# Performance work log

Hardware: AMD Instinct MI355X
Metric: run time of the kernel (lower is better)

## Reference

```python
import jax, jax.numpy as jnp
import numpy as np

B, S, H, NH = 2, 2048, 2048, 16
HD = H // NH
SCALE = 1.0 / np.sqrt(HD).astype(np.float32)


def setup_inputs() -> dict:
    key = jax.random.key(0)
    ks = jax.random.split(key, 11)
    std = 1.0 / np.sqrt(H)
    inp = {
        'query': jax.random.normal(ks[0], (B, S, H), dtype=jnp.float32),
        'key': jax.random.normal(ks[1], (B, S, H), dtype=jnp.float32),
        'value': jax.random.normal(ks[2], (B, S, H), dtype=jnp.float32),
        'Wq': jax.random.normal(ks[3], (H, H), dtype=jnp.float32) * std,
        'bq': jax.random.normal(ks[4], (H,), dtype=jnp.float32) * std,
        'Wk': jax.random.normal(ks[5], (H, H), dtype=jnp.float32) * std,
        'bk': jax.random.normal(ks[6], (H,), dtype=jnp.float32) * std,
        'Wv': jax.random.normal(ks[7], (H, H), dtype=jnp.float32) * std,
        'bv': jax.random.normal(ks[8], (H,), dtype=jnp.float32) * std,
        'Wo': jax.random.normal(ks[9], (H, H), dtype=jnp.float32) * std,
        'bo': jax.random.normal(ks[10], (H,), dtype=jnp.float32) * std,
    }
    return inp


def reference(query, key, value, Wq, bq, Wk, bk, Wv, bv, Wo, bo):
    # Linear projections (torch Linear: x @ W.T + b)
    q = query @ Wq.T + bq
    k = key @ Wk.T + bk
    v = value @ Wv.T + bv
    # [B, NH, S, HD]
    q = q.reshape(B, S, NH, HD).transpose(0, 2, 1, 3)
    k = k.reshape(B, S, NH, HD).transpose(0, 2, 1, 3)
    v = v.reshape(B, S, NH, HD).transpose(0, 2, 1, 3)
    scores = jnp.einsum('bhqd,bhkd->bhqk', q, k) * SCALE
    attn = jax.nn.softmax(scores, axis=-1)  # dropout p=0 (eval)
    ctx = jnp.einsum('bhqk,bhkd->bhqd', attn, v)
    ctx = ctx.transpose(0, 2, 1, 3).reshape(B, S, H)
    out = ctx @ Wo.T + bo
    return out
```

## Files before the change

kernel.cpp:

```cpp
#include <hip/hip_runtime.h>


typedef __bf16 bf16_t;
typedef __bf16 bf16x8 __attribute__((ext_vector_type(8)));
typedef float  f32x4  __attribute__((ext_vector_type(4)));

#define DEVI __device__ __forceinline__

DEVI void async_copy16(const void* gsrc, void* ldst) {
  __builtin_amdgcn_global_load_lds(
      (const __attribute__((address_space(1))) unsigned int*)gsrc,
      (__attribute__((address_space(3))) unsigned int*)ldst, 16, 0, 0);
}

constexpr int Bc = 2, Sc = 2048, Hc = 2048, NHc = 16, HDc = 128;
constexpr float SCALE_F = 0.088388347648318447f;
constexpr int PSTR = 72;

DEVI void cast_body(const float* __restrict__ in, bf16_t* __restrict__ out) {
  int i = (blockIdx.x * 256 + threadIdx.x) * 8;
  float4 f0 = *(const float4*)(in + i);
  float4 f1 = *(const float4*)(in + i + 4);
  union { bf16_t h[8]; uint4 u; } o;
  o.h[0] = (bf16_t)f0.x; o.h[1] = (bf16_t)f0.y;
  o.h[2] = (bf16_t)f0.z; o.h[3] = (bf16_t)f0.w;
  o.h[4] = (bf16_t)f1.x; o.h[5] = (bf16_t)f1.y;
  o.h[6] = (bf16_t)f1.z; o.h[7] = (bf16_t)f1.w;
  *(uint4*)(out + i) = o.u;
}

__global__ void cast3(const float* __restrict__ a, const float* __restrict__ b,
                      const float* __restrict__ c, bf16_t* __restrict__ oa,
                      bf16_t* __restrict__ ob, bf16_t* __restrict__ oc) {
  const float* src = blockIdx.y == 0 ? a : blockIdx.y == 1 ? b : c;
  bf16_t* dst = blockIdx.y == 0 ? oa : blockIdx.y == 1 ? ob : oc;
  cast_body(src, dst);
}

__global__ void cast4(const float* __restrict__ a, const float* __restrict__ b,
                      const float* __restrict__ c, const float* __restrict__ d,
                      bf16_t* __restrict__ oa, bf16_t* __restrict__ ob,
                      bf16_t* __restrict__ oc, bf16_t* __restrict__ od) {
  const float* src = blockIdx.y == 0 ? a : blockIdx.y == 1 ? b
                   : blockIdx.y == 2 ? c : d;
  bf16_t* dst = blockIdx.y == 0 ? oa : blockIdx.y == 1 ? ob
              : blockIdx.y == 2 ? oc : od;
  cast_body(src, dst);
}

template <int M, int N, int K, int OUT_MODE>
__global__ __launch_bounds__(256, 2) void gemm_bt(const bf16_t* __restrict__ A,
                                                  const bf16_t* __restrict__ Bw,
                                                  const float* __restrict__ bias,
                                                  void* __restrict__ Cout,
                                                  float scale) {
  constexpr int BM = 128, BN = 128, BK = 64;
  __shared__ __align__(16) bf16_t As[BM * BK];
  __shared__ __align__(16) bf16_t Bs[BN * BK];
  const int tid = threadIdx.x;
  const int lane = tid & 63;
  const int wave = tid >> 6;
  const int bm = blockIdx.x & (M / BM - 1);
  const int bn = blockIdx.x / (M / BM);
  const int wm = wave >> 1, wn = wave & 1;
  const int quad = lane >> 4, l15 = lane & 15;

  int s_r[4], s_c[4];
#pragma unroll
  for (int i = 0; i < 4; ++i) {
    int seg = wave * 4 + i;
    int r = seg * 8 + (lane >> 3);
    s_r[i] = r;
    s_c[i] = (lane & 7) ^ (r & 7);
  }
  const bf16_t* Abase = A + (size_t)bm * BM * K;
  const bf16_t* Bbase = Bw + (size_t)bn * BN * K;

  f32x4 zero4 = {0.f, 0.f, 0.f, 0.f};
  f32x4 acc[4][4];
#pragma unroll
  for (int i = 0; i < 4; ++i)
#pragma unroll
    for (int j = 0; j < 4; ++j) acc[i][j] = zero4;

  int arow[4], brow[4];
#pragma unroll
  for (int t = 0; t < 4; ++t) {
    arow[t] = wm * 64 + t * 16 + l15;
    brow[t] = wn * 64 + t * 16 + l15;
  }

  for (int kt = 0; kt < K / BK; ++kt) {
    const int k0 = kt * BK;
#pragma unroll
    for (int i = 0; i < 4; ++i) {
      int seg = wave * 4 + i;
      async_copy16(Abase + (size_t)s_r[i] * K + k0 + s_c[i] * 8, As + seg * 512);
      async_copy16(Bbase + (size_t)s_r[i] * K + k0 + s_c[i] * 8, Bs + seg * 512);
    }
    __syncthreads();
#pragma unroll
    for (int ks = 0; ks < 2; ++ks) {
      bf16x8 af[4], bfv[4];
#pragma unroll
      for (int mt = 0; mt < 4; ++mt)
        af[mt] = *(const bf16x8*)(As + arow[mt] * 64 +
                                  (((ks * 4 + quad) ^ (arow[mt] & 7)) * 8));
#pragma unroll
      for (int nt = 0; nt < 4; ++nt)
        bfv[nt] = *(const bf16x8*)(Bs + brow[nt] * 64 +
                                   (((ks * 4 + quad) ^ (brow[nt] & 7)) * 8));
#pragma unroll
      for (int mt = 0; mt < 4; ++mt)
#pragma unroll
        for (int nt = 0; nt < 4; ++nt)
          acc[mt][nt] = __builtin_amdgcn_mfma_f32_16x16x32_bf16(
              af[mt], bfv[nt], acc[mt][nt], 0, 0, 0);
    }
    __syncthreads();
  }

  float bv[4];
#pragma unroll
  for (int nt = 0; nt < 4; ++nt) bv[nt] = bias[bn * BN + brow[nt]];

#pragma unroll
  for (int mt = 0; mt < 4; ++mt) {
    const int rbase = bm * BM + wm * 64 + mt * 16 + quad * 4;
#pragma unroll
    for (int nt = 0; nt < 4; ++nt) {
      const int col = bn * BN + brow[nt];
      if constexpr (OUT_MODE == 0) {
        bf16_t* C = (bf16_t*)Cout;
#pragma unroll
        for (int r = 0; r < 4; ++r)
          C[(size_t)(rbase + r) * N + col] = (bf16_t)((acc[mt][nt][r] + bv[nt]) * scale);
      } else if constexpr (OUT_MODE == 2) {
        float* C = (float*)Cout;
#pragma unroll
        for (int r = 0; r < 4; ++r)
          C[(size_t)(rbase + r) * N + col] = acc[mt][nt][r] + bv[nt];
      } else {
        bf16_t* C = (bf16_t*)Cout;
        const int bb = rbase >> 11;
        const int s0 = rbase & (Sc - 1);
        const int h = col >> 7, d = col & (HDc - 1);
        union { bf16_t h4[4]; uint2 u; } o;
#pragma unroll
        for (int r = 0; r < 4; ++r) o.h4[r] = (bf16_t)(acc[mt][nt][r] + bv[nt]);
        *(uint2*)(C + (((size_t)(bb * NHc + h) * HDc + d) * Sc + s0)) = o.u;
      }
    }
  }
}

__global__ __launch_bounds__(256, 2) void flash_attn(const bf16_t* __restrict__ Q,
                                                     const bf16_t* __restrict__ Kg,
                                                     const bf16_t* __restrict__ Vt,
                                                     bf16_t* __restrict__ ctx) {
  __shared__ __align__(16) bf16_t smem[64 * 128 + 128 * 64 + 4 * 32 * PSTR];
  bf16_t* Ks = smem;
  bf16_t* Vs = smem + 8192;
  bf16_t* Ps = smem + 16384;

  const int tid = threadIdx.x, lane = tid & 63, wave = tid >> 6;
  const int quad = lane >> 4, l15 = lane & 15;
  const int bid = blockIdx.x;
  const int qt = bid & 15, h = (bid >> 4) & 15, b = bid >> 8;

  bf16_t* Pw = Ps + wave * (32 * PSTR);

  bf16x8 qf[2][4];
#pragma unroll
  for (int mt = 0; mt < 2; ++mt) {
    int grow = b * Sc + qt * 128 + wave * 32 + mt * 16 + l15;
    const bf16_t* qp = Q + (size_t)grow * Hc + h * HDc;
#pragma unroll
    for (int kc = 0; kc < 4; ++kc) qf[mt][kc] = *(const bf16x8*)(qp + kc * 32 + quad * 8);
  }

  f32x4 zero4 = {0.f, 0.f, 0.f, 0.f};
  f32x4 o[2][8];
#pragma unroll
  for (int mt = 0; mt < 2; ++mt)
#pragma unroll
    for (int dt = 0; dt < 8; ++dt) o[mt][dt] = zero4;
  float mrow[2][4], lrow[2][4];
#pragma unroll
  for (int mt = 0; mt < 2; ++mt)
#pragma unroll
    for (int r = 0; r < 4; ++r) { mrow[mt][r] = -1e30f; lrow[mt][r] = 0.f; }

  int kr_[4], kc_[4], vr_[4], vc_[4];
#pragma unroll
  for (int i = 0; i < 4; ++i) {
    int s = wave * 4 + i;
    kr_[i] = s * 4 + quad;        kc_[i] = l15 ^ (kr_[i] & 7);
    vr_[i] = s * 8 + (lane >> 3); vc_[i] = (lane & 7) ^ (vr_[i] & 7);
  }
  const bf16_t* Kbase = Kg + (size_t)b * Sc * Hc + h * HDc;
  const bf16_t* Vbase = Vt + (size_t)(b * NHc + h) * HDc * Sc;

  for (int kb = 0; kb < 32; ++kb) {
#pragma unroll
    for (int i = 0; i < 4; ++i) {
      int s = wave * 4 + i;
      async_copy16(Kbase + (size_t)(kb * 64 + kr_[i]) * Hc + kc_[i] * 8, Ks + s * 512);
      async_copy16(Vbase + (size_t)vr_[i] * Sc + kb * 64 + vc_[i] * 8, Vs + s * 512);
    }
    __syncthreads();

    f32x4 sf[2][4];
#pragma unroll
    for (int mt = 0; mt < 2; ++mt)
#pragma unroll
      for (int nt = 0; nt < 4; ++nt) sf[mt][nt] = zero4;
#pragma unroll
    for (int kc = 0; kc < 4; ++kc)
#pragma unroll
      for (int nt = 0; nt < 4; ++nt) {
        int kr = nt * 16 + l15;
        bf16x8 kf = *(const bf16x8*)(Ks + kr * 128 + (((kc * 4 + quad) ^ (kr & 7)) * 8));
        sf[0][nt] = __builtin_amdgcn_mfma_f32_16x16x32_bf16(qf[0][kc], kf, sf[0][nt], 0, 0, 0);
        sf[1][nt] = __builtin_amdgcn_mfma_f32_16x16x32_bf16(qf[1][kc], kf, sf[1][nt], 0, 0, 0);
      }

#pragma unroll
    for (int mt = 0; mt < 2; ++mt)
#pragma unroll
      for (int r = 0; r < 4; ++r) {
        float mx = sf[mt][0][r];
#pragma unroll
        for (int nt = 1; nt < 4; ++nt) mx = fmaxf(mx, sf[mt][nt][r]);
#pragma unroll
        for (int off = 1; off < 16; off <<= 1) mx = fmaxf(mx, __shfl_xor(mx, off));
        float mnew = fmaxf(mrow[mt][r], mx);
        float alpha = __expf(mrow[mt][r] - mnew);
        float rs = 0.f;
#pragma unroll
        for (int nt = 0; nt < 4; ++nt) {
          float p = __expf(sf[mt][nt][r] - mnew);
          sf[mt][nt][r] = p;
          rs += p;
        }
#pragma unroll
        for (int off = 1; off < 16; off <<= 1) rs += __shfl_xor(rs, off);
        lrow[mt][r] = lrow[mt][r] * alpha + rs;
        mrow[mt][r] = mnew;
#pragma unroll
        for (int dt = 0; dt < 8; ++dt) o[mt][dt][r] *= alpha;
      }

#pragma unroll
    for (int mt = 0; mt < 2; ++mt)
#pragma unroll
      for (int nt = 0; nt < 4; ++nt)
#pragma unroll
        for (int r = 0; r < 4; ++r)
          Pw[(mt * 16 + quad * 4 + r) * PSTR + nt * 16 + l15] = (bf16_t)sf[mt][nt][r];

    bf16x8 pf[2][2];
#pragma unroll
    for (int mt = 0; mt < 2; ++mt) {
      const bf16_t* pr = Pw + (mt * 16 + l15) * PSTR;
#pragma unroll
      for (int kc = 0; kc < 2; ++kc)
        pf[mt][kc] = *(const bf16x8*)(pr + kc * 32 + quad * 8);
    }

#pragma unroll
    for (int kc = 0; kc < 2; ++kc)
#pragma unroll
      for (int dt = 0; dt < 8; ++dt) {
        int vr = dt * 16 + l15;
        bf16x8 vf = *(const bf16x8*)(Vs + vr * 64 + (((kc * 4 + quad) ^ (vr & 7)) * 8));
        o[0][dt] = __builtin_amdgcn_mfma_f32_16x16x32_bf16(pf[0][kc], vf, o[0][dt], 0, 0, 0);
        o[1][dt] = __builtin_amdgcn_mfma_f32_16x16x32_bf16(pf[1][kc], vf, o[1][dt], 0, 0, 0);
      }
    __syncthreads();
  }

  __syncthreads();
  bf16_t* Ow = smem + wave * 4096;
#pragma unroll
  for (int mt = 0; mt < 2; ++mt) {
    float rinv[4];
#pragma unroll
    for (int r = 0; r < 4; ++r) rinv[r] = 1.f / lrow[mt][r];
#pragma unroll
    for (int dt = 0; dt < 8; ++dt)
#pragma unroll
      for (int r = 0; r < 4; ++r)
        Ow[(mt * 16 + quad * 4 + r) * 128 + dt * 16 + l15] = (bf16_t)(o[mt][dt][r] * rinv[r]);
  }
#pragma unroll
  for (int r = 0; r < 32; ++r) {
    unsigned v = *(const unsigned*)(Ow + r * 128 + lane * 2);
    int grow = b * Sc + qt * 128 + wave * 32 + r;
    *(unsigned*)(ctx + (size_t)grow * Hc + h * HDc + lane * 2) = v;
  }
}

extern "C" void kernel_launch(void* const* d_in, const int* in_sizes, int n_in,
                              void* d_out, int out_size, void* d_ws, size_t ws_size,
                              hipStream_t stream) {
  const float* query = (const float*)d_in[0];
  const float* key_i = (const float*)d_in[1];
  const float* value = (const float*)d_in[2];
  const float* Wq = (const float*)d_in[3];
  const float* bq = (const float*)d_in[4];
  const float* Wk = (const float*)d_in[5];
  const float* bk = (const float*)d_in[6];
  const float* Wv = (const float*)d_in[7];
  const float* bv = (const float*)d_in[8];
  const float* Wo = (const float*)d_in[9];
  const float* bo = (const float*)d_in[10];

  const size_t XE = (size_t)Bc * Sc * Hc;
  const size_t WE = (size_t)Hc * Hc;
  const size_t need = 6 * XE * 2 + 4 * WE * 2;
  if (ws_size < need) return;

  char* ws = (char*)d_ws;
  size_t off = 0;
  auto alloc = [&](size_t bytes) {
    char* p = ws + off;
    off += (bytes + 255) & ~(size_t)255;
    return p;
  };
  bf16_t* Xq = (bf16_t*)alloc(XE * 2);
  bf16_t* Xk = (bf16_t*)alloc(XE * 2);
  bf16_t* Xv = (bf16_t*)alloc(XE * 2);
  bf16_t* Wqb = (bf16_t*)alloc(WE * 2);
  bf16_t* Wkb = (bf16_t*)alloc(WE * 2);
  bf16_t* Wvb = (bf16_t*)alloc(WE * 2);
  bf16_t* Wob = (bf16_t*)alloc(WE * 2);
  bf16_t* qb = (bf16_t*)alloc(XE * 2);
  bf16_t* kb = (bf16_t*)alloc(XE * 2);
  bf16_t* vtb = (bf16_t*)alloc(XE * 2);
  bf16_t* ctxb = Xq;

  cast3<<<dim3((unsigned)(XE / 2048), 3), 256, 0, stream>>>(query, key_i, value, Xq, Xk, Xv);
  cast4<<<dim3((unsigned)(WE / 2048), 4), 256, 0, stream>>>(Wq, Wk, Wv, Wo, Wqb, Wkb, Wvb, Wob);

  gemm_bt<4096, 2048, 2048, 0><<<512, 256, 0, stream>>>(Xq, Wqb, bq, qb, SCALE_F);
  gemm_bt<4096, 2048, 2048, 0><<<512, 256, 0, stream>>>(Xk, Wkb, bk, kb, 1.0f);
  gemm_bt<4096, 2048, 2048, 1><<<512, 256, 0, stream>>>(Xv, Wvb, bv, vtb, 1.0f);

  flash_attn<<<512, 256, 0, stream>>>(qb, kb, vtb, ctxb);

  gemm_bt<4096, 2048, 2048, 2><<<512, 256, 0, stream>>>(ctxb, Wob, bo, (float*)d_out, 1.0f);
}
```

Baseline: 479.0 us.

## Pipeline projection GEMMs with triple-buffered LDS and larger 256x128 tiles

```diff
diff --git a/kernel.cpp b/kernel.cpp
--- a/kernel.cpp
+++ b/kernel.cpp
@@ -49,14 +49,16 @@
 }
 
 template <int M, int N, int K, int OUT_MODE>
-__global__ __launch_bounds__(256, 2) void gemm_bt(const bf16_t* __restrict__ A,
+__global__ __launch_bounds__(512, 2) void gemm_bt(const bf16_t* __restrict__ A,
                                                   const bf16_t* __restrict__ Bw,
                                                   const float* __restrict__ bias,
                                                   void* __restrict__ Cout,
                                                   float scale) {
-  constexpr int BM = 128, BN = 128, BK = 64;
-  __shared__ __align__(16) bf16_t As[BM * BK];
-  __shared__ __align__(16) bf16_t Bs[BN * BK];
+  constexpr int BM = 256, BN = 128, BK = 64;
+  constexpr int NT = K / BK;
+  constexpr int SLOT = (BM + BN) * BK;
+  __shared__ __align__(16) bf16_t lds[3 * SLOT];
+
   const int tid = threadIdx.x;
   const int lane = tid & 63;
   const int wave = tid >> 6;
@@ -65,16 +67,27 @@
   const int wm = wave >> 1, wn = wave & 1;
   const int quad = lane >> 4, l15 = lane & 15;
 
-  int s_r[4], s_c[4];
-#pragma unroll
-  for (int i = 0; i < 4; ++i) {
-    int seg = wave * 4 + i;
-    int r = seg * 8 + (lane >> 3);
-    s_r[i] = r;
-    s_c[i] = (lane & 7) ^ (r & 7);
-  }
   const bf16_t* Abase = A + (size_t)bm * BM * K;
   const bf16_t* Bbase = Bw + (size_t)bn * BN * K;
+  const bf16_t* asrc0; const bf16_t* asrc1; const bf16_t* asrc2; const bf16_t* asrc3;
+  const bf16_t* bsrc0; const bf16_t* bsrc1;
+  int aoff0, aoff1, aoff2, aoff3, boff0, boff1;
+  {
+    int i0 = wave * 4;
+    int r0 = i0 * 8 + (lane >> 3);       aoff0 = i0 * 512;
+    int r1 = (i0 + 1) * 8 + (lane >> 3); aoff1 = (i0 + 1) * 512;
+    int r2 = (i0 + 2) * 8 + (lane >> 3); aoff2 = (i0 + 2) * 512;
+    int r3 = (i0 + 3) * 8 + (lane >> 3); aoff3 = (i0 + 3) * 512;
+    asrc0 = Abase + (size_t)r0 * K + (((lane & 7) ^ (r0 & 7)) * 8);
+    asrc1 = Abase + (size_t)r1 * K + (((lane & 7) ^ (r1 & 7)) * 8);
+    asrc2 = Abase + (size_t)r2 * K + (((lane & 7) ^ (r2 & 7)) * 8);
+    asrc3 = Abase + (size_t)r3 * K + (((lane & 7) ^ (r3 & 7)) * 8);
+    int j0 = wave * 2;
+    int s0 = j0 * 8 + (lane >> 3);       boff0 = BM * BK + j0 * 512;
+    int s1 = (j0 + 1) * 8 + (lane >> 3); boff1 = BM * BK + (j0 + 1) * 512;
+    bsrc0 = Bbase + (size_t)s0 * K + (((lane & 7) ^ (s0 & 7)) * 8);
+    bsrc1 = Bbase + (size_t)s1 * K + (((lane & 7) ^ (s1 & 7)) * 8);
+  }
 
   f32x4 zero4 = {0.f, 0.f, 0.f, 0.f};
   f32x4 acc[4][4];
@@ -90,17 +103,43 @@
     brow[t] = wn * 64 + t * 16 + l15;
   }
 
-  for (int kt = 0; kt < K / BK; ++kt) {
-    const int k0 = kt * BK;
-#pragma unroll
-    for (int i = 0; i < 4; ++i) {
-      int seg = wave * 4 + i;
-      async_copy16(Abase + (size_t)s_r[i] * K + k0 + s_c[i] * 8, As + seg * 512);
-      async_copy16(Bbase + (size_t)s_r[i] * K + k0 + s_c[i] * 8, Bs + seg * 512);
-    }
-    __syncthreads();
+  auto stage_half0 = [&](int kt) {
+    bf16_t* slot = lds + (kt % 3) * SLOT;
+    int k0 = kt * BK;
+    async_copy16(asrc0 + k0, slot + aoff0);
+    async_copy16(asrc1 + k0, slot + aoff1);
+    async_copy16(bsrc0 + k0, slot + boff0);
+  };
+  auto stage_half1 = [&](int kt) {
+    bf16_t* slot = lds + (kt % 3) * SLOT;
+    int k0 = kt * BK;
+    async_copy16(asrc2 + k0, slot + aoff2);
+    async_copy16(asrc3 + k0, slot + aoff3);
+    async_copy16(bsrc1 + k0, slot + boff1);
+  };
+
+  stage_half0(0); stage_half1(0);
+  stage_half0(1); stage_half1(1);
+
+  for (int kt = 0; kt < NT; ++kt) {
+    if (kt + 1 < NT) {
+      asm volatile("s_waitcnt vmcnt(6)" ::: "memory");
+    } else {
+      asm volatile("s_waitcnt vmcnt(0)" ::: "memory");
+    }
+    __builtin_amdgcn_s_barrier();
+    asm volatile("" ::: "memory");
+
+    const bf16_t* As = lds + (kt % 3) * SLOT;
+    const bf16_t* Bs = As + BM * BK;
+    const bool do_stage = (kt + 2 < NT);
+
 #pragma unroll
     for (int ks = 0; ks < 2; ++ks) {
+      if (do_stage) {
+        if (ks == 0) stage_half0(kt + 2);
+        else         stage_half1(kt + 2);
+      }
       bf16x8 af[4], bfv[4];
 #pragma unroll
       for (int mt = 0; mt < 4; ++mt)
@@ -110,14 +149,15 @@
       for (int nt = 0; nt < 4; ++nt)
         bfv[nt] = *(const bf16x8*)(Bs + brow[nt] * 64 +
                                    (((ks * 4 + quad) ^ (brow[nt] & 7)) * 8));
+      __builtin_amdgcn_s_setprio(1);
 #pragma unroll
       for (int mt = 0; mt < 4; ++mt)
 #pragma unroll
         for (int nt = 0; nt < 4; ++nt)
           acc[mt][nt] = __builtin_amdgcn_mfma_f32_16x16x32_bf16(
               af[mt], bfv[nt], acc[mt][nt], 0, 0, 0);
-    }
-    __syncthreads();
+      __builtin_amdgcn_s_setprio(0);
+    }
   }
 
   float bv[4];
@@ -343,11 +383,11 @@
   cast3<<<dim3((unsigned)(XE / 2048), 3), 256, 0, stream>>>(query, key_i, value, Xq, Xk, Xv);
   cast4<<<dim3((unsigned)(WE / 2048), 4), 256, 0, stream>>>(Wq, Wk, Wv, Wo, Wqb, Wkb, Wvb, Wob);
 
-  gemm_bt<4096, 2048, 2048, 0><<<512, 256, 0, stream>>>(Xq, Wqb, bq, qb, SCALE_F);
-  gemm_bt<4096, 2048, 2048, 0><<<512, 256, 0, stream>>>(Xk, Wkb, bk, kb, 1.0f);
-  gemm_bt<4096, 2048, 2048, 1><<<512, 256, 0, stream>>>(Xv, Wvb, bv, vtb, 1.0f);
+  gemm_bt<4096, 2048, 2048, 0><<<256, 512, 0, stream>>>(Xq, Wqb, bq, qb, SCALE_F);
+  gemm_bt<4096, 2048, 2048, 0><<<256, 512, 0, stream>>>(Xk, Wkb, bk, kb, 1.0f);
+  gemm_bt<4096, 2048, 2048, 1><<<256, 512, 0, stream>>>(Xv, Wvb, bv, vtb, 1.0f);
 
   flash_attn<<<512, 256, 0, stream>>>(qb, kb, vtb, ctxb);
 
-  gemm_bt<4096, 2048, 2048, 2><<<512, 256, 0, stream>>>(ctxb, Wob, bo, (float*)d_out, 1.0f);
-}
+  gemm_bt<4096, 2048, 2048, 2><<<256, 512, 0, stream>>>(ctxb, Wob, bo, (float*)d_out, 1.0f);
+}
```

After: 474.4 us. Within noise of the previous version (-1.0%).
